# Performance work log

Hardware: AMD Instinct MI355X
Metric: run time of the kernel (lower is better)

The kernel has to match this reference:

```python
import jax, jax.numpy as jnp
import numpy as np

B, N, M = 8, 256, 256
C_IN, C_MID, C_OUT = 64, 256, 256


def setup_inputs() -> dict:
    key = jax.random.key(0)
    k1, k2, k3, k4 = jax.random.split(key, 4)
    x = jax.random.normal(k1, (B, N, M, C_IN), dtype=jnp.float32)
    # nn.Linear(in_channels, mid_channels): weight (mid, in), bias (mid)
    w1 = jax.random.normal(k2, (C_MID, C_IN), dtype=jnp.float32) * (1.0 / np.sqrt(C_IN))
    b1 = jax.random.normal(k3, (C_MID,), dtype=jnp.float32) * 0.01
    # nn.Linear(in+mid, out, bias=False): weight (out, in+mid)
    w2 = jax.random.normal(k4, (C_OUT, C_IN + C_MID), dtype=jnp.float32) * (1.0 / np.sqrt(C_IN + C_MID))
    return {"x": x, "w1": w1, "b1": b1, "w2": w2, "dim_target": 2}


def reference(x, w1, b1, w2, dim_target):
    # first_process: Linear over last dim -> (B, N, M, C_MID)
    z = jnp.einsum('bnmc,dc->bnmd', x, w1) + b1
    # MaxPoolingAggregator: max over dim_target keepdim, then expand back over M
    z_vertex = jnp.max(z, axis=dim_target, keepdims=True)  # (B, N, 1, C_MID)
    z_vertex = jnp.broadcast_to(z_vertex, z.shape)          # (B, N, M, C_MID)
    # ConcatMerger(dim_feature=-1): cat edge features x with vertex features
    merged = jnp.concatenate([x, z_vertex], axis=-1)        # (B, N, M, C_IN+C_MID)
    # second_process: bias-free Linear -> (B, N, M, C_OUT)
    return jnp.einsum('bnmc,dc->bnmd', merged, w2)
```

## Files before the change

kernel.cpp:

```cpp
#include <hip/hip_runtime.h>


#define CIN  64
#define KPAD 72
#define PLANE 18432

typedef __attribute__((ext_vector_type(8))) short short8;
typedef __attribute__((ext_vector_type(4))) float float4v;

__device__ __forceinline__ short f2bf(float f) {
    union { float f; unsigned u; } c; c.f = f;
    unsigned u = c.u;
    unsigned r = (u + 0x7FFFu + ((u >> 16) & 1u)) >> 16;
    return (short)r;
}
__device__ __forceinline__ float bf2f(short s) {
    union { unsigned u; float f; } c;
    c.u = ((unsigned)(unsigned short)s) << 16;
    return c.f;
}

__global__ void prep_weights(const float* __restrict__ w1,
                             const float* __restrict__ w2,
                             short* __restrict__ wsS) {
    int i = blockIdx.x * 256 + threadIdx.x;
    if (i < 16384) {
        float f = w1[i];
        short h = f2bf(f);
        wsS[i] = h;
        wsS[16384 + i] = f2bf(f - bf2f(h));
    } else if (i < 32768) {
        int q = i - 16384;
        int j = q >> 6, k = q & 63;
        float f = w2[j * 320 + k];
        short h = f2bf(f);
        wsS[32768 + q] = h;
        wsS[49152 + q] = f2bf(f - bf2f(h));
    } else if (i < 98304) {
        int q = i - 32768;
        int d = q >> 8, j = q & 255;
        ((float*)(wsS + 65536))[q] = w2[j * 320 + 64 + d];
    }
}

__global__ __launch_bounds__(256, 2)
void fused_pointnet(const float* __restrict__ x,
                    const float* __restrict__ b1,
                    const short* __restrict__ w1p,
                    const short* __restrict__ w2xp,
                    const float* __restrict__ w2zt,
                    float* __restrict__ out) {
    __shared__ short wlds[2 * PLANE];
    __shared__ float red[1024];
    __shared__ float zv[256];
    __shared__ float vv[256];

    const int tid = threadIdx.x;
    const int bn  = blockIdx.x;
    const int w   = tid >> 6;
    const int l   = tid & 63;
    const int dl  = l & 15;
    const int q   = l >> 4;
    const int mw  = w * 64;
    const float* __restrict__ xg = x + (size_t)bn * (256 * CIN);

    float4 xa0[4][2], xa1[4][2];
#pragma unroll
    for (int t = 0; t < 4; ++t)
#pragma unroll
        for (int s = 0; s < 2; ++s) {
            const float* p = xg + (mw + t * 16 + dl) * CIN + s * 32 + q * 8;
            xa0[t][s] = *(const float4*)p;
            xa1[t][s] = *(const float4*)(p + 4);
        }

    {
        const short8* src = (const short8*)w1p;
#pragma unroll
        for (int it = 0; it < 16; ++it) {
            int i = tid + 256 * it;
            int plane = i >> 11;
            int c = i & 2047;
            int row = c >> 3, k = (c & 7) << 3;
            *(short8*)&wlds[plane * PLANE + row * KPAD + k] = src[i];
        }
    }

    short8 ahi[4][2], alo[4][2];
#pragma unroll
    for (int t = 0; t < 4; ++t)
#pragma unroll
        for (int s = 0; s < 2; ++s) {
            float e[8];
            e[0] = xa0[t][s].x; e[1] = xa0[t][s].y; e[2] = xa0[t][s].z; e[3] = xa0[t][s].w;
            e[4] = xa1[t][s].x; e[5] = xa1[t][s].y; e[6] = xa1[t][s].z; e[7] = xa1[t][s].w;
#pragma unroll
            for (int j = 0; j < 8; ++j) {
                short h = f2bf(e[j]);
                ahi[t][s][j] = h;
                alo[t][s][j] = f2bf(e[j] - bf2f(h));
            }
        }
    __syncthreads();

#pragma unroll
    for (int chunk = 0; chunk < 4; ++chunk) {
        const int d0c = chunk * 64;
        short8 bhi[4][2], blo[4][2];
#pragma unroll
        for (int dt = 0; dt < 4; ++dt)
#pragma unroll
            for (int s = 0; s < 2; ++s) {
                int off = (d0c + dt * 16 + dl) * KPAD + s * 32 + q * 8;
                bhi[dt][s] = *(const short8*)&wlds[off];
                blo[dt][s] = *(const short8*)&wlds[off + PLANE];
            }
        float4v acc[4][4];
#pragma unroll
        for (int t = 0; t < 4; ++t)
#pragma unroll
            for (int dt = 0; dt < 4; ++dt) {
                float4v a = {0.f, 0.f, 0.f, 0.f};
#pragma unroll
                for (int s = 0; s < 2; ++s) {
                    a = __builtin_amdgcn_mfma_f32_16x16x32_bf16(ahi[t][s], bhi[dt][s], a, 0, 0, 0);
                    a = __builtin_amdgcn_mfma_f32_16x16x32_bf16(ahi[t][s], blo[dt][s], a, 0, 0, 0);
                    a = __builtin_amdgcn_mfma_f32_16x16x32_bf16(alo[t][s], bhi[dt][s], a, 0, 0, 0);
                }
                acc[t][dt] = a;
            }
#pragma unroll
        for (int dt = 0; dt < 4; ++dt) {
            float mx = -3.0e38f;
#pragma unroll
            for (int t = 0; t < 4; ++t)
#pragma unroll
                for (int r = 0; r < 4; ++r) mx = fmaxf(mx, acc[t][dt][r]);
            mx = fmaxf(mx, __shfl_xor(mx, 16));
            mx = fmaxf(mx, __shfl_xor(mx, 32));
            if (q == 0) red[w * 256 + d0c + dt * 16 + dl] = mx;
        }
    }
    __syncthreads();
    zv[tid] = fmaxf(fmaxf(red[tid], red[256 + tid]),
                    fmaxf(red[512 + tid], red[768 + tid])) + b1[tid];
    __syncthreads();

    {
        const short8* src = (const short8*)w2xp;
#pragma unroll
        for (int it = 0; it < 16; ++it) {
            int i = tid + 256 * it;
            int plane = i >> 11;
            int c = i & 2047;
            int row = c >> 3, k = (c & 7) << 3;
            *(short8*)&wlds[plane * PLANE + row * KPAD + k] = src[i];
        }
    }
    {
        const int jq = tid & 63;
        const int dpart = tid >> 6;
        const float4* wz4 = (const float4*)w2zt;
        float4 vacc = make_float4(0.f, 0.f, 0.f, 0.f);
#pragma unroll 4
        for (int d = 0; d < 64; ++d) {
            int dd = dpart * 64 + d;
            float s = zv[dd];
            float4 wv = wz4[dd * 64 + jq];
            vacc.x = fmaf(s, wv.x, vacc.x);
            vacc.y = fmaf(s, wv.y, vacc.y);
            vacc.z = fmaf(s, wv.z, vacc.z);
            vacc.w = fmaf(s, wv.w, vacc.w);
        }
        ((float4*)red)[dpart * 64 + jq] = vacc;
    }
    __syncthreads();
    vv[tid] = red[tid] + red[256 + tid] + red[512 + tid] + red[768 + tid];
    __syncthreads();

    float* __restrict__ og = out + (size_t)bn * (256 * 256);
#pragma unroll
    for (int chunk = 0; chunk < 4; ++chunk) {
        const int d0c = chunk * 64;
        short8 bhi[4][2], blo[4][2];
#pragma unroll
        for (int dt = 0; dt < 4; ++dt)
#pragma unroll
            for (int s = 0; s < 2; ++s) {
                int off = (d0c + dt * 16 + dl) * KPAD + s * 32 + q * 8;
                bhi[dt][s] = *(const short8*)&wlds[off];
                blo[dt][s] = *(const short8*)&wlds[off + PLANE];
            }
        float vdt[4];
#pragma unroll
        for (int dt = 0; dt < 4; ++dt) vdt[dt] = vv[d0c + dt * 16 + dl];
#pragma unroll
        for (int t = 0; t < 4; ++t)
#pragma unroll
            for (int dt = 0; dt < 4; ++dt) {
                float4v a = {0.f, 0.f, 0.f, 0.f};
#pragma unroll
                for (int s = 0; s < 2; ++s) {
                    a = __builtin_amdgcn_mfma_f32_16x16x32_bf16(ahi[t][s], bhi[dt][s], a, 0, 0, 0);
                    a = __builtin_amdgcn_mfma_f32_16x16x32_bf16(ahi[t][s], blo[dt][s], a, 0, 0, 0);
                    a = __builtin_amdgcn_mfma_f32_16x16x32_bf16(alo[t][s], bhi[dt][s], a, 0, 0, 0);
                }
                const int rowb = (mw + t * 16 + q * 4) * 256 + d0c + dt * 16 + dl;
#pragma unroll
                for (int r = 0; r < 4; ++r)
                    og[rowb + r * 256] = a[r] + vdt[dt];
            }
    }
}

extern "C" void kernel_launch(void* const* d_in, const int* in_sizes, int n_in,
                              void* d_out, int out_size, void* d_ws, size_t ws_size,
                              hipStream_t stream) {
    const float* x  = (const float*)d_in[0];
    const float* w1 = (const float*)d_in[1];
    const float* b1 = (const float*)d_in[2];
    const float* w2 = (const float*)d_in[3];
    short* wsS = (short*)d_ws;
    float* out = (float*)d_out;

    hipLaunchKernelGGL(prep_weights, dim3(384), dim3(256), 0, stream, w1, w2, wsS);
    hipLaunchKernelGGL(fused_pointnet, dim3(2048), dim3(256), 0, stream,
                       x, b1, wsS, wsS + 32768, (const float*)(wsS + 65536), out);
}
```

Baseline: 642.1 us.

## Split fused kernel into vertex-max kernel and output GEMM kernel

The single fused kernel becomes two. The first computes the per-(b,n) max-pooled vertex vector and its projection through w2, using 512 threads and reading w1 straight from global memory instead of staging it in LDS. The second computes the output GEMM over half-row blocks, with w2x staged in LDS and the precomputed vertex term added. The aim is higher occupancy and less register pressure by splitting the work and dropping the w1 LDS stage. The cost is reading x twice, an extra launch, and an intermediate buffer in workspace.

```diff
diff --git a/kernel.cpp b/kernel.cpp
--- a/kernel.cpp
+++ b/kernel.cpp
@@ -43,57 +43,34 @@
     }
 }
 
-__global__ __launch_bounds__(256, 2)
-void fused_pointnet(const float* __restrict__ x,
-                    const float* __restrict__ b1,
-                    const short* __restrict__ w1p,
-                    const short* __restrict__ w2xp,
-                    const float* __restrict__ w2zt,
-                    float* __restrict__ out) {
-    __shared__ short wlds[2 * PLANE];
-    __shared__ float red[1024];
+__global__ __launch_bounds__(512, 4)
+void pointnet_v(const float* __restrict__ x,
+                const float* __restrict__ b1,
+                const short* __restrict__ w1p,
+                const float* __restrict__ w2zt,
+                float* __restrict__ vout) {
+    __shared__ float red[2048];
     __shared__ float zv[256];
-    __shared__ float vv[256];
-
     const int tid = threadIdx.x;
     const int bn  = blockIdx.x;
     const int w   = tid >> 6;
     const int l   = tid & 63;
     const int dl  = l & 15;
     const int q   = l >> 4;
-    const int mw  = w * 64;
+    const int mw  = w * 32;
     const float* __restrict__ xg = x + (size_t)bn * (256 * CIN);
 
-    float4 xa0[4][2], xa1[4][2];
-#pragma unroll
-    for (int t = 0; t < 4; ++t)
+    short8 ahi[2][2], alo[2][2];
+#pragma unroll
+    for (int t = 0; t < 2; ++t)
 #pragma unroll
         for (int s = 0; s < 2; ++s) {
             const float* p = xg + (mw + t * 16 + dl) * CIN + s * 32 + q * 8;
-            xa0[t][s] = *(const float4*)p;
-            xa1[t][s] = *(const float4*)(p + 4);
-        }
-
-    {
-        const short8* src = (const short8*)w1p;
-#pragma unroll
-        for (int it = 0; it < 16; ++it) {
-            int i = tid + 256 * it;
-            int plane = i >> 11;
-            int c = i & 2047;
-            int row = c >> 3, k = (c & 7) << 3;
-            *(short8*)&wlds[plane * PLANE + row * KPAD + k] = src[i];
-        }
-    }
-
-    short8 ahi[4][2], alo[4][2];
-#pragma unroll
-    for (int t = 0; t < 4; ++t)
-#pragma unroll
-        for (int s = 0; s < 2; ++s) {
+            float4 x0 = *(const float4*)p;
+            float4 x1 = *(const float4*)(p + 4);
             float e[8];
-            e[0] = xa0[t][s].x; e[1] = xa0[t][s].y; e[2] = xa0[t][s].z; e[3] = xa0[t][s].w;
-            e[4] = xa1[t][s].x; e[5] = xa1[t][s].y; e[6] = xa1[t][s].z; e[7] = xa1[t][s].w;
+            e[0] = x0.x; e[1] = x0.y; e[2] = x0.z; e[3] = x0.w;
+            e[4] = x1.x; e[5] = x1.y; e[6] = x1.z; e[7] = x1.w;
 #pragma unroll
             for (int j = 0; j < 8; ++j) {
                 short h = f2bf(e[j]);
@@ -101,70 +78,48 @@
                 alo[t][s][j] = f2bf(e[j] - bf2f(h));
             }
         }
-    __syncthreads();
-
-#pragma unroll
-    for (int chunk = 0; chunk < 4; ++chunk) {
-        const int d0c = chunk * 64;
-        short8 bhi[4][2], blo[4][2];
-#pragma unroll
-        for (int dt = 0; dt < 4; ++dt)
-#pragma unroll
-            for (int s = 0; s < 2; ++s) {
-                int off = (d0c + dt * 16 + dl) * KPAD + s * 32 + q * 8;
-                bhi[dt][s] = *(const short8*)&wlds[off];
-                blo[dt][s] = *(const short8*)&wlds[off + PLANE];
-            }
-        float4v acc[4][4];
-#pragma unroll
-        for (int t = 0; t < 4; ++t)
-#pragma unroll
-            for (int dt = 0; dt < 4; ++dt) {
-                float4v a = {0.f, 0.f, 0.f, 0.f};
-#pragma unroll
-                for (int s = 0; s < 2; ++s) {
-                    a = __builtin_amdgcn_mfma_f32_16x16x32_bf16(ahi[t][s], bhi[dt][s], a, 0, 0, 0);
-                    a = __builtin_amdgcn_mfma_f32_16x16x32_bf16(ahi[t][s], blo[dt][s], a, 0, 0, 0);
-                    a = __builtin_amdgcn_mfma_f32_16x16x32_bf16(alo[t][s], bhi[dt][s], a, 0, 0, 0);
-                }
-                acc[t][dt] = a;
-            }
-#pragma unroll
-        for (int dt = 0; dt < 4; ++dt) {
-            float mx = -3.0e38f;
-#pragma unroll
-            for (int t = 0; t < 4; ++t)
-#pragma unroll
-                for (int r = 0; r < 4; ++r) mx = fmaxf(mx, acc[t][dt][r]);
-            mx = fmaxf(mx, __shfl_xor(mx, 16));
-            mx = fmaxf(mx, __shfl_xor(mx, 32));
-            if (q == 0) red[w * 256 + d0c + dt * 16 + dl] = mx;
-        }
-    }
-    __syncthreads();
-    zv[tid] = fmaxf(fmaxf(red[tid], red[256 + tid]),
-                    fmaxf(red[512 + tid], red[768 + tid])) + b1[tid];
-    __syncthreads();
-
-    {
-        const short8* src = (const short8*)w2xp;
-#pragma unroll
-        for (int it = 0; it < 16; ++it) {
-            int i = tid + 256 * it;
-            int plane = i >> 11;
-            int c = i & 2047;
-            int row = c >> 3, k = (c & 7) << 3;
-            *(short8*)&wlds[plane * PLANE + row * KPAD + k] = src[i];
-        }
-    }
+
+#pragma unroll 2
+    for (int dt = 0; dt < 16; ++dt) {
+        const short* bp = w1p + (dt * 16 + dl) * CIN + q * 8;
+        short8 bh0 = *(const short8*)bp;
+        short8 bh1 = *(const short8*)(bp + 32);
+        short8 bl0 = *(const short8*)(bp + 16384);
+        short8 bl1 = *(const short8*)(bp + 16384 + 32);
+        float mx = -3.0e38f;
+#pragma unroll
+        for (int t = 0; t < 2; ++t) {
+            float4v a = {0.f, 0.f, 0.f, 0.f};
+            a = __builtin_amdgcn_mfma_f32_16x16x32_bf16(ahi[t][0], bh0, a, 0, 0, 0);
+            a = __builtin_amdgcn_mfma_f32_16x16x32_bf16(ahi[t][0], bl0, a, 0, 0, 0);
+            a = __builtin_amdgcn_mfma_f32_16x16x32_bf16(alo[t][0], bh0, a, 0, 0, 0);
+            a = __builtin_amdgcn_mfma_f32_16x16x32_bf16(ahi[t][1], bh1, a, 0, 0, 0);
+            a = __builtin_amdgcn_mfma_f32_16x16x32_bf16(ahi[t][1], bl1, a, 0, 0, 0);
+            a = __builtin_amdgcn_mfma_f32_16x16x32_bf16(alo[t][1], bh1, a, 0, 0, 0);
+            mx = fmaxf(mx, fmaxf(fmaxf(a[0], a[1]), fmaxf(a[2], a[3])));
+        }
+        mx = fmaxf(mx, __shfl_xor(mx, 16));
+        mx = fmaxf(mx, __shfl_xor(mx, 32));
+        if (q == 0) red[w * 256 + dt * 16 + dl] = mx;
+    }
+    __syncthreads();
+    if (tid < 256) {
+        float m0 = fmaxf(red[tid], red[256 + tid]);
+        float m1 = fmaxf(red[512 + tid], red[768 + tid]);
+        float m2 = fmaxf(red[1024 + tid], red[1280 + tid]);
+        float m3 = fmaxf(red[1536 + tid], red[1792 + tid]);
+        zv[tid] = fmaxf(fmaxf(m0, m1), fmaxf(m2, m3)) + b1[tid];
+    }
+    __syncthreads();
+
     {
         const int jq = tid & 63;
         const int dpart = tid >> 6;
         const float4* wz4 = (const float4*)w2zt;
         float4 vacc = make_float4(0.f, 0.f, 0.f, 0.f);
 #pragma unroll 4
-        for (int d = 0; d < 64; ++d) {
-            int dd = dpart * 64 + d;
+        for (int d = 0; d < 32; ++d) {
+            int dd = dpart * 32 + d;
             float s = zv[dd];
             float4 wv = wz4[dd * 64 + jq];
             vacc.x = fmaf(s, wv.x, vacc.x);
@@ -175,41 +130,81 @@
         ((float4*)red)[dpart * 64 + jq] = vacc;
     }
     __syncthreads();
-    vv[tid] = red[tid] + red[256 + tid] + red[512 + tid] + red[768 + tid];
-    __syncthreads();
-
-    float* __restrict__ og = out + (size_t)bn * (256 * 256);
-#pragma unroll
-    for (int chunk = 0; chunk < 4; ++chunk) {
-        const int d0c = chunk * 64;
-        short8 bhi[4][2], blo[4][2];
-#pragma unroll
-        for (int dt = 0; dt < 4; ++dt)
-#pragma unroll
-            for (int s = 0; s < 2; ++s) {
-                int off = (d0c + dt * 16 + dl) * KPAD + s * 32 + q * 8;
-                bhi[dt][s] = *(const short8*)&wlds[off];
-                blo[dt][s] = *(const short8*)&wlds[off + PLANE];
-            }
-        float vdt[4];
-#pragma unroll
-        for (int dt = 0; dt < 4; ++dt) vdt[dt] = vv[d0c + dt * 16 + dl];
-#pragma unroll
-        for (int t = 0; t < 4; ++t)
-#pragma unroll
-            for (int dt = 0; dt < 4; ++dt) {
-                float4v a = {0.f, 0.f, 0.f, 0.f};
-#pragma unroll
-                for (int s = 0; s < 2; ++s) {
-                    a = __builtin_amdgcn_mfma_f32_16x16x32_bf16(ahi[t][s], bhi[dt][s], a, 0, 0, 0);
-                    a = __builtin_amdgcn_mfma_f32_16x16x32_bf16(ahi[t][s], blo[dt][s], a, 0, 0, 0);
-                    a = __builtin_amdgcn_mfma_f32_16x16x32_bf16(alo[t][s], bhi[dt][s], a, 0, 0, 0);
-                }
-                const int rowb = (mw + t * 16 + q * 4) * 256 + d0c + dt * 16 + dl;
-#pragma unroll
-                for (int r = 0; r < 4; ++r)
-                    og[rowb + r * 256] = a[r] + vdt[dt];
-            }
+    if (tid < 256) {
+        float s = red[tid] + red[256 + tid] + red[512 + tid] + red[768 + tid]
+                + red[1024 + tid] + red[1280 + tid] + red[1536 + tid] + red[1792 + tid];
+        vout[(size_t)bn * 256 + tid] = s;
+    }
+}
+
+__global__ __launch_bounds__(512, 4)
+void pointnet_out(const float* __restrict__ x,
+                  const short* __restrict__ w2xp,
+                  const float* __restrict__ vin,
+                  float* __restrict__ out) {
+    __shared__ short wlds[2 * PLANE];
+    __shared__ float vsh[256];
+
+    const int tid  = threadIdx.x;
+    const int bn   = blockIdx.x >> 1;
+    const int half = blockIdx.x & 1;
+    const int l    = tid & 63;
+    const int dl   = l & 15;
+    const int q    = l >> 4;
+    const int row0 = half * 128 + (tid >> 6) * 16;
+
+    {
+        const short8* src = (const short8*)w2xp;
+#pragma unroll
+        for (int it = 0; it < 8; ++it) {
+            int i = tid + 512 * it;
+            int plane = i >> 11;
+            int c = i & 2047;
+            int row = c >> 3, k = (c & 7) << 3;
+            *(short8*)&wlds[plane * PLANE + row * KPAD + k] = src[i];
+        }
+    }
+    if (tid < 256) vsh[tid] = vin[(size_t)bn * 256 + tid];
+
+    const float* __restrict__ xg = x + (size_t)bn * (256 * CIN);
+    short8 ahi[2], alo[2];
+#pragma unroll
+    for (int s = 0; s < 2; ++s) {
+        const float* p = xg + (row0 + dl) * CIN + s * 32 + q * 8;
+        float4 x0 = *(const float4*)p;
+        float4 x1 = *(const float4*)(p + 4);
+        float e[8];
+        e[0] = x0.x; e[1] = x0.y; e[2] = x0.z; e[3] = x0.w;
+        e[4] = x1.x; e[5] = x1.y; e[6] = x1.z; e[7] = x1.w;
+#pragma unroll
+        for (int j = 0; j < 8; ++j) {
+            short h = f2bf(e[j]);
+            ahi[s][j] = h;
+            alo[s][j] = f2bf(e[j] - bf2f(h));
+        }
+    }
+    __syncthreads();
+
+    float* __restrict__ og = out + (size_t)bn * 65536 + (size_t)row0 * 256;
+#pragma unroll 2
+    for (int dt = 0; dt < 16; ++dt) {
+        const int off = (dt * 16 + dl) * KPAD + q * 8;
+        short8 bh0 = *(const short8*)&wlds[off];
+        short8 bh1 = *(const short8*)&wlds[off + 32];
+        short8 bl0 = *(const short8*)&wlds[off + PLANE];
+        short8 bl1 = *(const short8*)&wlds[off + PLANE + 32];
+        float4v a = {0.f, 0.f, 0.f, 0.f};
+        a = __builtin_amdgcn_mfma_f32_16x16x32_bf16(ahi[0], bh0, a, 0, 0, 0);
+        a = __builtin_amdgcn_mfma_f32_16x16x32_bf16(ahi[0], bl0, a, 0, 0, 0);
+        a = __builtin_amdgcn_mfma_f32_16x16x32_bf16(alo[0], bh0, a, 0, 0, 0);
+        a = __builtin_amdgcn_mfma_f32_16x16x32_bf16(ahi[1], bh1, a, 0, 0, 0);
+        a = __builtin_amdgcn_mfma_f32_16x16x32_bf16(ahi[1], bl1, a, 0, 0, 0);
+        a = __builtin_amdgcn_mfma_f32_16x16x32_bf16(alo[1], bh1, a, 0, 0, 0);
+        const float vd = vsh[dt * 16 + dl];
+        const int cb = (q * 4) * 256 + dt * 16 + dl;
+#pragma unroll
+        for (int r = 0; r < 4; ++r)
+            og[cb + r * 256] = a[r] + vd;
     }
 }
 
@@ -223,7 +218,12 @@
     short* wsS = (short*)d_ws;
     float* out = (float*)d_out;
 
+    const float* w2zt = (const float*)(wsS + 65536);
+    float* vbuf = (float*)((char*)d_ws + 393216);
+
     hipLaunchKernelGGL(prep_weights, dim3(384), dim3(256), 0, stream, w1, w2, wsS);
-    hipLaunchKernelGGL(fused_pointnet, dim3(2048), dim3(256), 0, stream,
-                       x, b1, wsS, wsS + 32768, (const float*)(wsS + 65536), out);
-}
+    hipLaunchKernelGGL(pointnet_v, dim3(2048), dim3(512), 0, stream,
+                       x, b1, wsS, w2zt, vbuf);
+    hipLaunchKernelGGL(pointnet_out, dim3(4096), dim3(512), 0, stream,
+                       x, wsS + 32768, vbuf, out);
+}
```

New measurement: 786.0 us. 1.22x slower.
